# Kernel optimization log

Hardware: AMD Instinct MI355X
Metric: run time of the kernel (lower is better)

## Reference

```python
import jax, jax.numpy as jnp
import numpy as np

CLASSES_WEIGHT = jnp.array([1.0, 1.0, 1.0], dtype=jnp.float32)  # default for num_classes==3
EPS = 0.0001


def setup_inputs() -> dict:
    key = jax.random.key(0)
    k1, k2 = jax.random.split(key)
    B, C = 4096, 3
    source = jax.random.normal(k1, (B, C), dtype=jnp.float32)
    target = jax.random.randint(k2, (B,), 0, C, dtype=jnp.int64)
    return {"source": source, "target": target}


def reference(source, target):
    B, C = source.shape
    n2 = B * B
    # new_target = clamp(one_hot, 1e-4, 1.0) * classes_weight (weights are 1.0)
    T = jnp.clip(jax.nn.one_hot(target, C, dtype=jnp.float32), EPS, 1.0)
    T = T * CLASSES_WEIGHT[None, :]
    # new_source = softmax(logits)
    S = jax.nn.softmax(source, axis=1)
    LS = jnp.log(S)
    LT = jnp.log(T)
    sS = jnp.sum(S * LS, axis=-1)  # [B] sum_c s_ic log s_ic
    sT = jnp.sum(T * LT, axis=-1)  # [B]
    # L0: mean cross-entropy of new_target against softmax probs
    loss_0 = jnp.mean(-jnp.sum(T * LS, axis=-1))
    # L1: a_ij = -sum s_i (log s_j - log s_i) = sS_i - S_i . LS_j ; same for target
    A1 = sS[:, None] - S @ LS.T  # [B,B]
    B1 = sT[:, None] - T @ LT.T
    loss_1 = (EPS + jnp.sum(jnp.abs(A1 - B1))) / n2
    # L2: a_ij = -sum t_j (log s_i - log t_j) = sT_j - LS_i . T_j
    A2 = sT[None, :] - LS @ T.T
    B2 = sT[None, :] - LT @ T.T
    loss_2 = (EPS + jnp.sum(jnp.abs(A2 - B2))) / n2
    # L3: a_ij = sS_i - S_i . LS_j (== A1); b_ij = sT_i - T_i . LS_j
    B3 = sT[:, None] - T @ LS.T
    loss_3 = (EPS + jnp.sum(jnp.abs(A1 - B3))) / n2
    total = (loss_0 + loss_1) + (loss_2 + loss_3)
    return total, loss_0, loss_1, loss_2, loss_3
```

## Files before the change

### kernel.cpp

```cpp
#include <hip/hip_runtime.h>
#include <math.h>

#define BN   4096
#define GX   16
#define GY   32
#define TJ   128
#define NB   (GX * GY)

#define LOGE  (-9.210340371976184f)
#define EPSF  (1e-4f)
#define STC   (2.0f * EPSF * LOGE)

__global__ __launch_bounds__(256) void k_pairs(const float* __restrict__ src,
                                               const int* __restrict__ tgt,
                                               float* __restrict__ partial) {
    __shared__ float4 js[TJ];
    __shared__ int    sc[3];
    int tid = threadIdx.x;
    int bx = blockIdx.x, by = blockIdx.y;

    if (tid < 3) sc[tid] = 0;

    int i = bx * 256 + tid;
    float S0, S1, S2, aI, sumLS_i, L0i, L1i, L2i;
    int ti;
    {
        float x0 = src[3*i], x1 = src[3*i+1], x2 = src[3*i+2];
        float m  = fmaxf(x0, fmaxf(x1, x2));
        float e0 = expf(x0 - m), e1 = expf(x1 - m), e2 = expf(x2 - m);
        float s  = e0 + e1 + e2;
        float inv = 1.0f / s;
        S0 = e0 * inv; S1 = e1 * inv; S2 = e2 * inv;
        float ls = logf(s);
        L0i = x0 - m - ls; L1i = x1 - m - ls; L2i = x2 - m - ls;
        sumLS_i = L0i + L1i + L2i;
        float sS = S0 * L0i + S1 * L1i + S2 * L2i;
        ti = tgt[i];
        aI = sS - STC;
    }
    float tif = (float)ti;
    float tdSame = aI + 2.0f * EPSF * LOGE;
    float tdDiff = aI + (1.0f + EPSF) * LOGE;
    float w0 = EPSF + ((ti == 0) ? (1.0f - EPSF) : 0.0f);
    float w1 = EPSF + ((ti == 1) ? (1.0f - EPSF) : 0.0f);
    float w2 = EPSF + ((ti == 2) ? (1.0f - EPSF) : 0.0f);
    float base = EPSF * (2.0f * LOGE - sumLS_i);
    float au0 = fabsf(base + (1.0f - EPSF) * (((ti == 0) ? 0.f : LOGE) - L0i));
    float au1 = fabsf(base + (1.0f - EPSF) * (((ti == 1) ? 0.f : LOGE) - L1i));
    float au2 = fabsf(base + (1.0f - EPSF) * (((ti == 2) ? 0.f : LOGE) - L2i));
    float LSt = (ti == 0) ? L0i : ((ti == 1) ? L1i : L2i);
    float c0 = (by == 0) ? -(EPSF * sumLS_i + (1.0f - EPSF) * LSt) : 0.0f;

    __syncthreads();

    if (tid < TJ) {
        int j = by * TJ + tid;
        float x0 = src[3*j], x1 = src[3*j+1], x2 = src[3*j+2];
        float m  = fmaxf(x0, fmaxf(x1, x2));
        float e0 = expf(x0 - m), e1 = expf(x1 - m), e2 = expf(x2 - m);
        float s  = e0 + e1 + e2;
        float ls = logf(s);
        int tj = tgt[j];
        js[tid] = make_float4(x0 - m - ls, x1 - m - ls, x2 - m - ls, (float)tj);
        atomicAdd(&sc[tj], 1);
    }
    __syncthreads();

    float c2 = (float)sc[0] * au0 + (float)sc[1] * au1 + (float)sc[2] * au2;

    float a1 = 0.f, a3 = 0.f;
    #pragma unroll 4
    for (int k = 0; k < TJ; ++k) {
        float4 L = js[k];
        float d   = fmaf(S0, L.x, fmaf(S1, L.y, S2 * L.z));
        float tls = fmaf(w0, L.x, fmaf(w1, L.y, w2 * L.z));
        float td  = (L.w == tif) ? tdSame : tdDiff;
        a1 += fabsf(td - d);
        a3 += fabsf(aI + tls - d);
    }

    __shared__ float r1[256], r3[256], r2[256], r0[256];
    r1[tid] = a1; r3[tid] = a3; r2[tid] = c2; r0[tid] = c0;
    __syncthreads();
    for (int s = 128; s > 0; s >>= 1) {
        if (tid < s) {
            r1[tid] += r1[tid + s]; r3[tid] += r3[tid + s];
            r2[tid] += r2[tid + s]; r0[tid] += r0[tid + s];
        }
        __syncthreads();
    }
    if (tid == 0) {
        int bid = by * GX + bx;
        float4 p = make_float4(r1[0], r3[0], r2[0], r0[0]);
        *reinterpret_cast<float4*>(partial + bid * 4) = p;
    }
}

__global__ __launch_bounds__(512) void k_final(const float* __restrict__ partial,
                                               float* __restrict__ out) {
    __shared__ double s1[512], s3[512], s2[512], s0[512];
    int tid = threadIdx.x;
    float4 p = *reinterpret_cast<const float4*>(partial + tid * 4);
    s1[tid] = (double)p.x; s3[tid] = (double)p.y;
    s2[tid] = (double)p.z; s0[tid] = (double)p.w;
    __syncthreads();
    for (int s = 256; s > 0; s >>= 1) {
        if (tid < s) {
            s1[tid] += s1[tid + s]; s3[tid] += s3[tid + s];
            s2[tid] += s2[tid + s]; s0[tid] += s0[tid + s];
        }
        __syncthreads();
    }
    if (tid == 0) {
        double n2 = (double)BN * (double)BN;
        double l0 = s0[0] / (double)BN;
        double l1 = (1e-4 + s1[0]) / n2;
        double l2 = (1e-4 + s2[0]) / n2;
        double l3 = (1e-4 + s3[0]) / n2;
        out[0] = (float)((l0 + l1) + (l2 + l3));
        out[1] = (float)l0;
        out[2] = (float)l1;
        out[3] = (float)l2;
        out[4] = (float)l3;
    }
}

extern "C" void kernel_launch(void* const* d_in, const int* in_sizes, int n_in,
                              void* d_out, int out_size, void* d_ws, size_t ws_size,
                              hipStream_t stream) {
    const float* src = (const float*)d_in[0];
    const int*   tgt = (const int*)d_in[1];
    float*       out = (float*)d_out;
    float*   partial = (float*)d_ws;

    k_pairs<<<dim3(GX, GY), 256, 0, stream>>>(src, tgt, partial);
    k_final<<<1, 512, 0, stream>>>(partial, out);
}
```

Baseline: 16.49 us.

## Fuse final reduction into pair kernel via cooperative grid sync

Merges the two kernels into one cooperative launch: each block writes its partial sums, a grid-wide sync follows, and block (0,0) then does the final double-precision reduction. The block reduction moves from a shared-memory tree to wavefront shuffles, and the L3 term is folded algebraically into a single fma chain with precomputed (w - S) weights, with deeper unrolling. This removes a second kernel launch and the shared-memory tree passes, at the cost of a cooperative launch and a grid barrier across 512 blocks.

```diff
diff --git a/kernel.cpp b/kernel.cpp
--- a/kernel.cpp
+++ b/kernel.cpp
@@ -1,5 +1,8 @@
 #include <hip/hip_runtime.h>
+#include <hip/hip_cooperative_groups.h>
 #include <math.h>
+
+namespace cg = cooperative_groups;
 
 #define BN   4096
 #define GX   16
@@ -11,11 +14,13 @@
 #define EPSF  (1e-4f)
 #define STC   (2.0f * EPSF * LOGE)
 
-__global__ __launch_bounds__(256) void k_pairs(const float* __restrict__ src,
-                                               const int* __restrict__ tgt,
-                                               float* __restrict__ partial) {
+__global__ __launch_bounds__(256) void k_all(const float* __restrict__ src,
+                                             const int* __restrict__ tgt,
+                                             float* __restrict__ partial,
+                                             float* __restrict__ out) {
     __shared__ float4 js[TJ];
     __shared__ int    sc[3];
+    __shared__ float4 wred[4];
     int tid = threadIdx.x;
     int bx = blockIdx.x, by = blockIdx.y;
 
@@ -41,9 +46,9 @@
     float tif = (float)ti;
     float tdSame = aI + 2.0f * EPSF * LOGE;
     float tdDiff = aI + (1.0f + EPSF) * LOGE;
-    float w0 = EPSF + ((ti == 0) ? (1.0f - EPSF) : 0.0f);
-    float w1 = EPSF + ((ti == 1) ? (1.0f - EPSF) : 0.0f);
-    float w2 = EPSF + ((ti == 2) ? (1.0f - EPSF) : 0.0f);
+    float dw0 = EPSF + ((ti == 0) ? (1.0f - EPSF) : 0.0f) - S0;
+    float dw1 = EPSF + ((ti == 1) ? (1.0f - EPSF) : 0.0f) - S1;
+    float dw2 = EPSF + ((ti == 2) ? (1.0f - EPSF) : 0.0f) - S2;
     float base = EPSF * (2.0f * LOGE - sumLS_i);
     float au0 = fabsf(base + (1.0f - EPSF) * (((ti == 0) ? 0.f : LOGE) - L0i));
     float au1 = fabsf(base + (1.0f - EPSF) * (((ti == 1) ? 0.f : LOGE) - L1i));
@@ -69,59 +74,71 @@
     float c2 = (float)sc[0] * au0 + (float)sc[1] * au1 + (float)sc[2] * au2;
 
     float a1 = 0.f, a3 = 0.f;
-    #pragma unroll 4
+    #pragma unroll 8
     for (int k = 0; k < TJ; ++k) {
         float4 L = js[k];
         float d   = fmaf(S0, L.x, fmaf(S1, L.y, S2 * L.z));
-        float tls = fmaf(w0, L.x, fmaf(w1, L.y, w2 * L.z));
+        float e3  = fmaf(dw0, L.x, fmaf(dw1, L.y, fmaf(dw2, L.z, aI)));
         float td  = (L.w == tif) ? tdSame : tdDiff;
         a1 += fabsf(td - d);
-        a3 += fabsf(aI + tls - d);
+        a3 += fabsf(e3);
     }
 
-    __shared__ float r1[256], r3[256], r2[256], r0[256];
-    r1[tid] = a1; r3[tid] = a3; r2[tid] = c2; r0[tid] = c0;
+    for (int off = 32; off > 0; off >>= 1) {
+        a1 += __shfl_down(a1, off);
+        a3 += __shfl_down(a3, off);
+        c2 += __shfl_down(c2, off);
+        c0 += __shfl_down(c0, off);
+    }
+    int lane = tid & 63, wid = tid >> 6;
+    if (lane == 0) wred[wid] = make_float4(a1, a3, c2, c0);
     __syncthreads();
-    for (int s = 128; s > 0; s >>= 1) {
-        if (tid < s) {
-            r1[tid] += r1[tid + s]; r3[tid] += r3[tid + s];
-            r2[tid] += r2[tid + s]; r0[tid] += r0[tid + s];
+    if (tid == 0) {
+        float4 p = wred[0];
+        #pragma unroll
+        for (int w = 1; w < 4; ++w) {
+            p.x += wred[w].x; p.y += wred[w].y;
+            p.z += wred[w].z; p.w += wred[w].w;
         }
+        partial[4*(by * GX + bx) + 0] = p.x;
+        partial[4*(by * GX + bx) + 1] = p.y;
+        partial[4*(by * GX + bx) + 2] = p.z;
+        partial[4*(by * GX + bx) + 3] = p.w;
+    }
+
+    cg::this_grid().sync();
+    if (bx == 0 && by == 0) {
+        double s1 = 0, s3 = 0, s2 = 0, s0d = 0;
+        for (int p = tid; p < NB; p += 256) {
+            float4 v = reinterpret_cast<const float4*>(partial)[p];
+            s1 += (double)v.x; s3 += (double)v.y;
+            s2 += (double)v.z; s0d += (double)v.w;
+        }
+        for (int off = 32; off > 0; off >>= 1) {
+            s1  += __shfl_down(s1, off);
+            s3  += __shfl_down(s3, off);
+            s2  += __shfl_down(s2, off);
+            s0d += __shfl_down(s0d, off);
+        }
+        __shared__ double d1[4], d3[4], d2[4], d0[4];
+        if (lane == 0) { d1[wid] = s1; d3[wid] = s3; d2[wid] = s2; d0[wid] = s0d; }
         __syncthreads();
-    }
-    if (tid == 0) {
-        int bid = by * GX + bx;
-        float4 p = make_float4(r1[0], r3[0], r2[0], r0[0]);
-        *reinterpret_cast<float4*>(partial + bid * 4) = p;
-    }
-}
-
-__global__ __launch_bounds__(512) void k_final(const float* __restrict__ partial,
-                                               float* __restrict__ out) {
-    __shared__ double s1[512], s3[512], s2[512], s0[512];
-    int tid = threadIdx.x;
-    float4 p = *reinterpret_cast<const float4*>(partial + tid * 4);
-    s1[tid] = (double)p.x; s3[tid] = (double)p.y;
-    s2[tid] = (double)p.z; s0[tid] = (double)p.w;
-    __syncthreads();
-    for (int s = 256; s > 0; s >>= 1) {
-        if (tid < s) {
-            s1[tid] += s1[tid + s]; s3[tid] += s3[tid + s];
-            s2[tid] += s2[tid + s]; s0[tid] += s0[tid + s];
+        if (tid == 0) {
+            double t1 = d1[0]+d1[1]+d1[2]+d1[3];
+            double t3 = d3[0]+d3[1]+d3[2]+d3[3];
+            double t2 = d2[0]+d2[1]+d2[2]+d2[3];
+            double t0 = d0[0]+d0[1]+d0[2]+d0[3];
+            double n2 = (double)BN * (double)BN;
+            double l0 = t0 / (double)BN;
+            double l1 = (1e-4 + t1) / n2;
+            double l2 = (1e-4 + t2) / n2;
+            double l3 = (1e-4 + t3) / n2;
+            out[0] = (float)((l0 + l1) + (l2 + l3));
+            out[1] = (float)l0;
+            out[2] = (float)l1;
+            out[3] = (float)l2;
+            out[4] = (float)l3;
         }
-        __syncthreads();
-    }
-    if (tid == 0) {
-        double n2 = (double)BN * (double)BN;
-        double l0 = s0[0] / (double)BN;
-        double l1 = (1e-4 + s1[0]) / n2;
-        double l2 = (1e-4 + s2[0]) / n2;
-        double l3 = (1e-4 + s3[0]) / n2;
-        out[0] = (float)((l0 + l1) + (l2 + l3));
-        out[1] = (float)l0;
-        out[2] = (float)l1;
-        out[3] = (float)l2;
-        out[4] = (float)l3;
     }
 }
 
@@ -133,6 +150,7 @@
     float*       out = (float*)d_out;
     float*   partial = (float*)d_ws;
 
-    k_pairs<<<dim3(GX, GY), 256, 0, stream>>>(src, tgt, partial);
-    k_final<<<1, 512, 0, stream>>>(partial, out);
+    void* args[] = { (void*)&src, (void*)&tgt, (void*)&partial, (void*)&out };
+    hipLaunchCooperativeKernel((const void*)k_all, dim3(GX, GY), dim3(256),
+                               args, 0, stream);
 }
```

New measurement: 54.36 us. +229.7%, slower.

## Bucket j-tile by target class, vectorize pair loop with packed f32x2, shuffle-reduce

Applied to the files above, without the earlier changes.

Sorts the per-block j tile into class segments in SoA shared arrays, so the same/different-target constant is uniform per segment and the per-element compare is gone. The inner loop is rewritten with packed two-wide float FMAs and max(x,-x) abs, reading float4 chunks and sharing the g term between the a1 and a3 sums. The shared-memory tree reduction is replaced with wavefront shuffles plus a small cross-wave combine. This adds extra barriers and shared atomics for the bucketing, plus scalar head/tail loops with some divergence.

```diff
diff --git a/kernel.cpp b/kernel.cpp
--- a/kernel.cpp
+++ b/kernel.cpp
@@ -11,18 +11,22 @@
 #define EPSF  (1e-4f)
 #define STC   (2.0f * EPSF * LOGE)
 
+typedef float f32x2 __attribute__((ext_vector_type(2)));
+__device__ __forceinline__ f32x2 sp(float v) { return (f32x2){v, v}; }
+
 __global__ __launch_bounds__(256) void k_pairs(const float* __restrict__ src,
                                                const int* __restrict__ tgt,
                                                float* __restrict__ partial) {
-    __shared__ float4 js[TJ];
-    __shared__ int    sc[3];
+    __shared__ float Lxs[TJ], Lys[TJ], Lzs[TJ];
+    __shared__ int   sc[3], off[3], rk[3];
+    __shared__ float4 wred[4];
     int tid = threadIdx.x;
     int bx = blockIdx.x, by = blockIdx.y;
 
-    if (tid < 3) sc[tid] = 0;
+    if (tid < 3) { sc[tid] = 0; rk[tid] = 0; }
 
     int i = bx * 256 + tid;
-    float S0, S1, S2, aI, sumLS_i, L0i, L1i, L2i;
+    float nS0, nS1, nS2, aI, sumLS_i, L0i, L1i, L2i;
     int ti;
     {
         float x0 = src[3*i], x1 = src[3*i+1], x2 = src[3*i+2];
@@ -30,17 +34,17 @@
         float e0 = expf(x0 - m), e1 = expf(x1 - m), e2 = expf(x2 - m);
         float s  = e0 + e1 + e2;
         float inv = 1.0f / s;
-        S0 = e0 * inv; S1 = e1 * inv; S2 = e2 * inv;
+        float S0 = e0 * inv, S1 = e1 * inv, S2 = e2 * inv;
         float ls = logf(s);
         L0i = x0 - m - ls; L1i = x1 - m - ls; L2i = x2 - m - ls;
         sumLS_i = L0i + L1i + L2i;
         float sS = S0 * L0i + S1 * L1i + S2 * L2i;
         ti = tgt[i];
         aI = sS - STC;
-    }
-    float tif = (float)ti;
-    float tdSame = aI + 2.0f * EPSF * LOGE;
-    float tdDiff = aI + (1.0f + EPSF) * LOGE;
+        nS0 = -S0; nS1 = -S1; nS2 = -S2;
+    }
+    float cSame = 2.0f * EPSF * LOGE;
+    float cDiff = (1.0f + EPSF) * LOGE;
     float w0 = EPSF + ((ti == 0) ? (1.0f - EPSF) : 0.0f);
     float w1 = EPSF + ((ti == 1) ? (1.0f - EPSF) : 0.0f);
     float w2 = EPSF + ((ti == 2) ? (1.0f - EPSF) : 0.0f);
@@ -53,6 +57,8 @@
 
     __syncthreads();
 
+    int tj = -1;
+    float jL0 = 0.f, jL1 = 0.f, jL2 = 0.f;
     if (tid < TJ) {
         int j = by * TJ + tid;
         float x0 = src[3*j], x1 = src[3*j+1], x2 = src[3*j+2];
@@ -60,38 +66,96 @@
         float e0 = expf(x0 - m), e1 = expf(x1 - m), e2 = expf(x2 - m);
         float s  = e0 + e1 + e2;
         float ls = logf(s);
-        int tj = tgt[j];
-        js[tid] = make_float4(x0 - m - ls, x1 - m - ls, x2 - m - ls, (float)tj);
+        jL0 = x0 - m - ls; jL1 = x1 - m - ls; jL2 = x2 - m - ls;
+        tj = tgt[j];
         atomicAdd(&sc[tj], 1);
     }
     __syncthreads();
+    if (tid == 0) { off[0] = 0; off[1] = sc[0]; off[2] = sc[0] + sc[1]; }
+    __syncthreads();
+    if (tid < TJ) {
+        int r = atomicAdd(&rk[tj], 1);
+        int pos = off[tj] + r;
+        Lxs[pos] = jL0; Lys[pos] = jL1; Lzs[pos] = jL2;
+    }
+    __syncthreads();
 
     float c2 = (float)sc[0] * au0 + (float)sc[1] * au1 + (float)sc[2] * au2;
 
-    float a1 = 0.f, a3 = 0.f;
-    #pragma unroll 4
-    for (int k = 0; k < TJ; ++k) {
-        float4 L = js[k];
-        float d   = fmaf(S0, L.x, fmaf(S1, L.y, S2 * L.z));
-        float tls = fmaf(w0, L.x, fmaf(w1, L.y, w2 * L.z));
-        float td  = (L.w == tif) ? tdSame : tdDiff;
-        a1 += fabsf(td - d);
-        a3 += fabsf(aI + tls - d);
-    }
-
-    __shared__ float r1[256], r3[256], r2[256], r0[256];
-    r1[tid] = a1; r3[tid] = a3; r2[tid] = c2; r0[tid] = c0;
-    __syncthreads();
-    for (int s = 128; s > 0; s >>= 1) {
-        if (tid < s) {
-            r1[tid] += r1[tid + s]; r3[tid] += r3[tid + s];
-            r2[tid] += r2[tid + s]; r0[tid] += r0[tid + s];
-        }
-        __syncthreads();
-    }
+    f32x2 nS0v = sp(nS0), nS1v = sp(nS1), nS2v = sp(nS2), aIv = sp(aI);
+    f32x2 w0v = sp(w0), w1v = sp(w1), w2v = sp(w2);
+    f32x2 acc1v = sp(0.f), acc3v = sp(0.f);
+    float a1s = 0.f, a3s = 0.f;
+
+    const float4* Lx4 = reinterpret_cast<const float4*>(Lxs);
+    const float4* Ly4 = reinterpret_cast<const float4*>(Lys);
+    const float4* Lz4 = reinterpret_cast<const float4*>(Lzs);
+
+    for (int s = 0; s < 3; ++s) {
+        int k   = off[s];
+        int end = k + sc[s];
+        float cseg = (s == ti) ? cSame : cDiff;
+        f32x2 cv = sp(cseg);
+        while (k < end && (k & 3)) {
+            float g = fmaf(nS0, Lxs[k], fmaf(nS1, Lys[k], fmaf(nS2, Lzs[k], aI)));
+            a1s += fabsf(g + cseg);
+            a3s += fabsf(fmaf(w0, Lxs[k], fmaf(w1, Lys[k], fmaf(w2, Lzs[k], g))));
+            ++k;
+        }
+        #pragma unroll 2
+        while (k + 3 < end) {
+            int p = k >> 2;
+            float4 qx = Lx4[p], qy = Ly4[p], qz = Lz4[p];
+            f32x2 lx, ly, lz, g, t, e;
+            lx = (f32x2){qx.x, qx.y}; ly = (f32x2){qy.x, qy.y}; lz = (f32x2){qz.x, qz.y};
+            g = __builtin_elementwise_fma(nS2v, lz, aIv);
+            g = __builtin_elementwise_fma(nS1v, ly, g);
+            g = __builtin_elementwise_fma(nS0v, lx, g);
+            t = g + cv;
+            acc1v += __builtin_elementwise_max(t, -t);
+            e = __builtin_elementwise_fma(w2v, lz, g);
+            e = __builtin_elementwise_fma(w1v, ly, e);
+            e = __builtin_elementwise_fma(w0v, lx, e);
+            acc3v += __builtin_elementwise_max(e, -e);
+            lx = (f32x2){qx.z, qx.w}; ly = (f32x2){qy.z, qy.w}; lz = (f32x2){qz.z, qz.w};
+            g = __builtin_elementwise_fma(nS2v, lz, aIv);
+            g = __builtin_elementwise_fma(nS1v, ly, g);
+            g = __builtin_elementwise_fma(nS0v, lx, g);
+            t = g + cv;
+            acc1v += __builtin_elementwise_max(t, -t);
+            e = __builtin_elementwise_fma(w2v, lz, g);
+            e = __builtin_elementwise_fma(w1v, ly, e);
+            e = __builtin_elementwise_fma(w0v, lx, e);
+            acc3v += __builtin_elementwise_max(e, -e);
+            k += 4;
+        }
+        while (k < end) {
+            float g = fmaf(nS0, Lxs[k], fmaf(nS1, Lys[k], fmaf(nS2, Lzs[k], aI)));
+            a1s += fabsf(g + cseg);
+            a3s += fabsf(fmaf(w0, Lxs[k], fmaf(w1, Lys[k], fmaf(w2, Lzs[k], g))));
+            ++k;
+        }
+    }
+    float a1 = acc1v.x + acc1v.y + a1s;
+    float a3 = acc3v.x + acc3v.y + a3s;
+
+    for (int o = 32; o > 0; o >>= 1) {
+        a1 += __shfl_down(a1, o);
+        a3 += __shfl_down(a3, o);
+        c2 += __shfl_down(c2, o);
+        c0 += __shfl_down(c0, o);
+    }
+    int lane = tid & 63, wid = tid >> 6;
+    if (lane == 0) wred[wid] = make_float4(a1, a3, c2, c0);
+    __syncthreads();
     if (tid == 0) {
+        float4 p = wred[0];
+        #pragma unroll
+        for (int w = 1; w < 4; ++w) {
+            p.x += wred[w].x; p.y += wred[w].y;
+            p.z += wred[w].z; p.w += wred[w].w;
+        }
         int bid = by * GX + bx;
-        float4 p = make_float4(r1[0], r3[0], r2[0], r0[0]);
         *reinterpret_cast<float4*>(partial + bid * 4) = p;
     }
 }
```

Measured after the change: 14.75 us, median of 2. -10.5%, faster.
